# Kernel tuning notes

Hardware: AMD Instinct MI355X
Metric: run time of the kernel (lower is better)

The kernel has to match this reference:

```python
import jax, jax.numpy as jnp
import numpy as np

DIM=2048; NH=16; QK_NOPE=128; QK_ROPE=64; QK_HD=QK_NOPE+QK_ROPE; V_HD=128
Q_LORA=1536; KV_LORA=512
IDX_NH=16; IDX_HD=128; IDX_TOPK=1024
B=1; S=2048
NEG=-1e30  # finite stand-in for -inf mask

def _hadamard(n):
    H=np.array([[1.0]],dtype=np.float32)
    while H.shape[0]<n:
        H=np.block([[H,H],[H,-H]])
    return H
_H=jnp.asarray(_hadamard(IDX_HD),jnp.bfloat16)  # symmetric Sylvester Hadamard

def _rope_tables(s,d):
    inv=1.0/(10000.0**(np.arange(0,d,2)/float(d)))
    ang=np.outer(np.arange(s),inv)
    return jnp.asarray(np.cos(ang),jnp.float32),jnp.asarray(np.sin(ang),jnp.float32)

def _rope_interleaved(x,cos,sin):
    # pairs (x[2i], x[2i+1]); x: (b,s,h,d), cos/sin: (s,d//2)
    x1=x[...,0::2]; x2=x[...,1::2]
    c=cos[None,:,None,:]; s_=sin[None,:,None,:]
    return jnp.stack([x1*c-x2*s_,x1*s_+x2*c],axis=-1).reshape(x.shape)

def _rope_half(x,cos,sin):
    # non-interleaved: pairs (x[i], x[i+d/2])
    d=x.shape[-1]//2
    x1=x[...,:d]; x2=x[...,d:]
    c=cos[None,:,None,:]; s_=sin[None,:,None,:]
    return jnp.concatenate([x1*c-x2*s_,x1*s_+x2*c],axis=-1)

def _rms(x,w,eps=1e-6):
    xf=x.astype(jnp.float32)
    xf=xf*jax.lax.rsqrt(jnp.mean(xf*xf,axis=-1,keepdims=True)+eps)
    return (w*xf).astype(x.dtype)

def _ln(x,w,b,eps=1e-6):
    xf=x.astype(jnp.float32)
    mu=jnp.mean(xf,axis=-1,keepdims=True)
    var=jnp.mean((xf-mu)**2,axis=-1,keepdims=True)
    return ((xf-mu)*jax.lax.rsqrt(var+eps)*w+b).astype(x.dtype)

def _rotate(x):
    # rotate_activation: bf16 Hadamard transform, x @ H * d^-0.5 (H symmetric)
    return (x.astype(jnp.bfloat16)@_H)*(IDX_HD**-0.5)

def _forward(x,start_pos,freqs_cos,freqs_sin,mask,q_a_proj,q_a_ln_w,q_b_proj,kv_a_proj,kv_a_ln_w,kv_b_proj,o_proj,idx_wq_b,idx_wk,idx_knorm_w,idx_knorm_b,idx_weights_proj):
    b,s,_=x.shape  # start_pos==0 prefill -> cache slice == current k/kv
    sm_scale=QK_HD**-0.5
    qr=_rms(x@q_a_proj.T,q_a_ln_w)                       # (b,s,q_lora)
    q=(qr@q_b_proj.T).reshape(b,s,NH,QK_HD)
    q_nope=q[...,:QK_NOPE]
    q_pe=_rope_interleaved(q[...,QK_NOPE:],freqs_cos,freqs_sin)
    kvp=x@kv_a_proj.T
    kv=_rms(kvp[...,:KV_LORA],kv_a_ln_w)                 # latent kv cache (b,t,c)
    k_pe=_rope_interleaved(kvp[...,KV_LORA:][:,:,None,:],freqs_cos,freqs_sin)[:,:,0,:]
    # ---------- Indexer ----------
    iq=(qr@idx_wq_b.T).reshape(b,s,IDX_NH,IDX_HD)
    iq=jnp.concatenate([_rope_half(iq[...,:QK_ROPE],freqs_cos,freqs_sin),iq[...,QK_ROPE:]],axis=-1)
    ik=_ln(x@idx_wk.T,idx_knorm_w,idx_knorm_b)           # (b,s,IDX_HD)
    ik=jnp.concatenate([_rope_half(ik[:,:,None,:QK_ROPE],freqs_cos,freqs_sin)[:,:,0,:],ik[...,QK_ROPE:]],axis=-1)
    iq=_rotate(iq); ik=_rotate(ik)                       # bf16 Hadamard-rotated
    iw=(x@idx_weights_proj.T)*(IDX_NH**-0.5)             # (b,s,hI)
    wq=(iw[...,None]*iq.astype(jnp.float32)*(IDX_HD**-0.5)).astype(jnp.bfloat16)
    sc=jnp.einsum('bshd,btd->bsht',wq,ik,preferred_element_type=jnp.float32)
    index_score=jax.nn.relu(sc).sum(axis=2)+mask[None]   # bf16_index: relu, head-sum
    _,topk=jax.lax.top_k(index_score,min(IDX_TOPK,s))    # (b,s,K)
    imask=jnp.full((b,s,s),jnp.float32(NEG))
    imask=imask.at[jnp.arange(b)[:,None,None],jnp.arange(s)[None,:,None],topk].set(0.0)
    imask=imask+mask[None]
    # ---------- Latent attention (absorbed) ----------
    wkv=kv_b_proj.reshape(NH,QK_NOPE+V_HD,KV_LORA)
    q_abs=jnp.einsum('bshd,hdc->bshc',q_nope,wkv[:,:QK_NOPE])
    scores=(jnp.einsum('bshc,btc->bsht',q_abs,kv)+jnp.einsum('bshr,btr->bsht',q_pe,k_pe))*sm_scale
    scores=scores+imask[:,:,None,:]
    p=jax.nn.softmax(scores.astype(jnp.float32),axis=-1).astype(x.dtype)
    o=jnp.einsum('bsht,btc->bshc',p,kv)
    o=jnp.einsum('bshc,hdc->bshd',o,wkv[:,QK_NOPE:])
    return o.reshape(b,s,NH*V_HD)@o_proj.T

def setup_inputs():
    key=jax.random.key(0)
    ks=jax.random.split(key,10)
    def w(k,shape):
        return jax.random.normal(k,shape,jnp.float32)*(shape[-1]**-0.5)
    cos,sin=_rope_tables(S,QK_ROPE)
    causal=jnp.where(jnp.triu(jnp.ones((S,S),bool),1),jnp.float32(NEG),jnp.float32(0.0))
    return {
        'x':jax.random.normal(ks[0],(B,S,DIM),jnp.float32),
        'start_pos':0,
        'freqs_cos':cos,'freqs_sin':sin,'mask':causal,
        'q_a_proj':w(ks[1],(Q_LORA,DIM)),
        'q_a_ln_w':jnp.ones((Q_LORA,),jnp.float32),
        'q_b_proj':w(ks[2],(NH*QK_HD,Q_LORA)),
        'kv_a_proj':w(ks[3],(KV_LORA+QK_ROPE,DIM)),
        'kv_a_ln_w':jnp.ones((KV_LORA,),jnp.float32),
        'kv_b_proj':w(ks[4],(NH*(QK_NOPE+V_HD),KV_LORA)),
        'o_proj':w(ks[5],(DIM,NH*V_HD)),
        'idx_wq_b':w(ks[6],(IDX_NH*IDX_HD,Q_LORA)),
        'idx_wk':w(ks[7],(IDX_HD,DIM)),
        'idx_knorm_w':jnp.ones((IDX_HD,),jnp.float32),
        'idx_knorm_b':jnp.zeros((IDX_HD,),jnp.float32),
        'idx_weights_proj':w(ks[8],(IDX_NH,DIM)),
    }

def reference(x,start_pos,freqs_cos,freqs_sin,mask,q_a_proj,q_a_ln_w,q_b_proj,kv_a_proj,kv_a_ln_w,kv_b_proj,o_proj,idx_wq_b,idx_wk,idx_knorm_w,idx_knorm_b,idx_weights_proj):
    return _forward(x,start_pos,freqs_cos,freqs_sin,mask,q_a_proj,q_a_ln_w,q_b_proj,kv_a_proj,kv_a_ln_w,kv_b_proj,o_proj,idx_wq_b,idx_wk,idx_knorm_w,idx_knorm_b,idx_weights_proj)
```

## Files before the change

### kernel.cpp

```cpp
#include <hip/hip_runtime.h>
#include <hip/hip_bf16.h>
#include <math.h>

#define S 2048
#define NH 16
#define DIM 2048
#define QK_NOPE 128
#define QK_ROPE 64
#define QK_HD 192
#define V_HD 128
#define Q_LORA 1536
#define KV_LORA 512
#define IDX_HD 128
#define SM_SCALE 0.07216878364870323f
#define SCHUNK 512
#define PADK 40
#define XPLD 2256
#define QLD 5120
#define XPLD_PAD 2304

typedef __hip_bfloat16 bf16;
typedef unsigned short ushort_t;
typedef __attribute__((ext_vector_type(8))) short short8;
typedef __attribute__((ext_vector_type(4))) float f32x4;

__device__ __forceinline__ f32x4 mfma_bf16(short8 a, short8 b, f32x4 c) {
    return __builtin_amdgcn_mfma_f32_16x16x32_bf16(a, b, c, 0, 0, 0);
}
__device__ __forceinline__ void async16(const void* g, void* l) {
    __builtin_amdgcn_global_load_lds((const __attribute__((address_space(1))) void*)g,
                                     (__attribute__((address_space(3))) void*)l, 16, 0, 0);
}
__device__ __forceinline__ unsigned short f2bf(float f) {
    unsigned int u = __float_as_uint(f);
    return (unsigned short)((u + 0x7fff + ((u >> 16) & 1)) >> 16);
}
__device__ __forceinline__ float bf2f(unsigned short b) {
    return __uint_as_float(((unsigned int)b) << 16);
}

__global__ __launch_bounds__(256) void split_kernel(const float* __restrict__ in, ushort_t* __restrict__ hi,
                                                    ushort_t* __restrict__ lo, int n4) {
    int idx = blockIdx.x * 256 + threadIdx.x;
    if (idx >= n4) return;
    float4 v = ((const float4*)in)[idx];
    ushort4 h, l;
    h.x = f2bf(v.x); l.x = f2bf(v.x - bf2f(h.x));
    h.y = f2bf(v.y); l.y = f2bf(v.y - bf2f(h.y));
    h.z = f2bf(v.z); l.z = f2bf(v.z - bf2f(h.z));
    h.w = f2bf(v.w); l.w = f2bf(v.w - bf2f(h.w));
    ((ushort4*)hi)[idx] = h;
    ((ushort4*)lo)[idx] = l;
}

__global__ __launch_bounds__(256) void splitw2_kernel(const float* __restrict__ kv_b,
                                                      ushort_t* __restrict__ w2h, ushort_t* __restrict__ w2l) {
    int idx = blockIdx.x * 256 + threadIdx.x;
    int h = idx >> 14, rem = idx & 16383;
    int row = rem >> 7, c4 = (rem & 127) * 4;
    float4 v = *(const float4*)(kv_b + ((size_t)(h * 256 + 128 + row)) * 512 + c4);
    ushort4 hh, ll;
    hh.x = f2bf(v.x); ll.x = f2bf(v.x - bf2f(hh.x));
    hh.y = f2bf(v.y); ll.y = f2bf(v.y - bf2f(hh.y));
    hh.z = f2bf(v.z); ll.z = f2bf(v.z - bf2f(hh.z));
    hh.w = f2bf(v.w); ll.w = f2bf(v.w - bf2f(hh.w));
    *(ushort4*)(w2h + ((size_t)(h * 128 + row)) * 512 + c4) = hh;
    *(ushort4*)(w2l + ((size_t)(h * 128 + row)) * 512 + c4) = ll;
}

__global__ __launch_bounds__(256) void gemm3_lds(const ushort_t* __restrict__ Ah, const ushort_t* __restrict__ Al,
                                                 const ushort_t* __restrict__ Bh, const ushort_t* __restrict__ Bl,
                                                 float* __restrict__ C, int M, int N, int K) {
    __shared__ ushort_t sAh[128 * 32], sAl[128 * 32], sBh[128 * 32], sBl[128 * 32];
    const int tid = threadIdx.x;
    const int bm = blockIdx.y * 128, bn = blockIdx.x * 128;
    const int w = tid >> 6, lane = tid & 63;
    const int wm = (w >> 1) * 64, wn = (w & 1) * 64;
    const int fr = lane & 15, fk = (lane >> 4) * 8;
    const int srow = tid >> 2, skc = (tid & 3) * 8;
    f32x4 acc[4][4];
    for (int i = 0; i < 4; ++i)
        for (int j = 0; j < 4; ++j) acc[i][j] = f32x4{0.f, 0.f, 0.f, 0.f};
    const ushort_t* pAh0 = Ah + (size_t)(bm + srow) * K + skc;
    const ushort_t* pAh1 = Ah + (size_t)(bm + 64 + srow) * K + skc;
    const ushort_t* pAl0 = Al + (size_t)(bm + srow) * K + skc;
    const ushort_t* pAl1 = Al + (size_t)(bm + 64 + srow) * K + skc;
    const ushort_t* pBh0 = Bh + (size_t)(bn + srow) * K + skc;
    const ushort_t* pBh1 = Bh + (size_t)(bn + 64 + srow) * K + skc;
    const ushort_t* pBl0 = Bl + (size_t)(bn + srow) * K + skc;
    const ushort_t* pBl1 = Bl + (size_t)(bn + 64 + srow) * K + skc;
    ushort_t* dA0 = &sAh[srow * 32 + skc];
    ushort_t* dA1 = &sAh[(64 + srow) * 32 + skc];
    ushort_t* dAl0 = &sAl[srow * 32 + skc];
    ushort_t* dAl1 = &sAl[(64 + srow) * 32 + skc];
    ushort_t* dB0 = &sBh[srow * 32 + skc];
    ushort_t* dB1 = &sBh[(64 + srow) * 32 + skc];
    ushort_t* dBl0 = &sBl[srow * 32 + skc];
    ushort_t* dBl1 = &sBl[(64 + srow) * 32 + skc];
    for (int k0 = 0; k0 < K; k0 += 32) {
        __syncthreads();
        async16(pAh0, dA0);  async16(pAh1, dA1);
        async16(pAl0, dAl0); async16(pAl1, dAl1);
        async16(pBh0, dB0);  async16(pBh1, dB1);
        async16(pBl0, dBl0); async16(pBl1, dBl1);
        pAh0 += 32; pAh1 += 32; pAl0 += 32; pAl1 += 32;
        pBh0 += 32; pBh1 += 32; pBl0 += 32; pBl1 += 32;
        __syncthreads();
        short8 ahf[4], alf[4], bhf[4], blf[4];
        for (int i = 0; i < 4; ++i) {
            int ro = (wm + i * 16 + fr) * 32 + fk;
            ahf[i] = *(const short8*)&sAh[ro];
            alf[i] = *(const short8*)&sAl[ro];
        }
        for (int j = 0; j < 4; ++j) {
            int ro = (wn + j * 16 + fr) * 32 + fk;
            bhf[j] = *(const short8*)&sBh[ro];
            blf[j] = *(const short8*)&sBl[ro];
        }
        for (int i = 0; i < 4; ++i)
            for (int j = 0; j < 4; ++j) {
                acc[i][j] = mfma_bf16(ahf[i], bhf[j], acc[i][j]);
                acc[i][j] = mfma_bf16(ahf[i], blf[j], acc[i][j]);
                acc[i][j] = mfma_bf16(alf[i], bhf[j], acc[i][j]);
            }
    }
    const int cr = (lane >> 4) * 4, cc = lane & 15;
    for (int i = 0; i < 4; ++i)
        for (int j = 0; j < 4; ++j) {
            int row = bm + wm + i * 16 + cr;
            int col = bn + wn + j * 16 + cc;
            if (col < N)
                for (int r = 0; r < 4; ++r)
                    C[(size_t)(row + r) * N + col] = acc[i][j][r];
        }
}

__global__ __launch_bounds__(256) void rms_kernel(const float* __restrict__ in, float* __restrict__ out,
                                                  const float* __restrict__ w, int C, int ldin, int ldout) {
    const int row = blockIdx.x;
    const float* xr = in + (size_t)row * ldin;
    float* yr = out + (size_t)row * ldout;
    float ss = 0.f;
    for (int c = threadIdx.x; c < C; c += 256) { float v = xr[c]; ss += v * v; }
    for (int o = 32; o; o >>= 1) ss += __shfl_down(ss, o, 64);
    __shared__ float red[4];
    const int wave = threadIdx.x >> 6, lane = threadIdx.x & 63;
    if (lane == 0) red[wave] = ss;
    __syncthreads();
    const float tot = red[0] + red[1] + red[2] + red[3];
    const float scale = rsqrtf(tot / (float)C + 1e-6f);
    for (int c = threadIdx.x; c < C; c += 256) yr[c] = w[c] * (xr[c] * scale);
}

__global__ __launch_bounds__(256) void rms_split_kernel(const float* __restrict__ in, ushort_t* __restrict__ hi,
                                                        ushort_t* __restrict__ lo, const float* __restrict__ w,
                                                        int C, int ldin) {
    const int row = blockIdx.x;
    const float* xr = in + (size_t)row * ldin;
    float ss = 0.f;
    for (int c = threadIdx.x; c < C; c += 256) { float v = xr[c]; ss += v * v; }
    for (int o = 32; o; o >>= 1) ss += __shfl_down(ss, o, 64);
    __shared__ float red[4];
    const int wave = threadIdx.x >> 6, lane = threadIdx.x & 63;
    if (lane == 0) red[wave] = ss;
    __syncthreads();
    const float tot = red[0] + red[1] + red[2] + red[3];
    const float scale = rsqrtf(tot / (float)C + 1e-6f);
    for (int c = threadIdx.x; c < C; c += 256) {
        float v = w[c] * (xr[c] * scale);
        unsigned short h = f2bf(v);
        hi[(size_t)row * C + c] = h;
        lo[(size_t)row * C + c] = f2bf(v - bf2f(h));
    }
}

__global__ __launch_bounds__(128) void ln_kernel(float* __restrict__ x, const float* __restrict__ w,
                                                 const float* __restrict__ b, int ld) {
    const int row = blockIdx.x;
    float* xr = x + (size_t)row * ld;
    const int tid = threadIdx.x;
    float v = xr[tid];
    float sm = v;
    for (int o = 32; o; o >>= 1) sm += __shfl_down(sm, o, 64);
    __shared__ float red[2];
    if ((tid & 63) == 0) red[tid >> 6] = sm;
    __syncthreads();
    const float mu = (red[0] + red[1]) * (1.f / 128.f);
    __syncthreads();
    float d = v - mu;
    float sv = d * d;
    for (int o = 32; o; o >>= 1) sv += __shfl_down(sv, o, 64);
    if ((tid & 63) == 0) red[tid >> 6] = sv;
    __syncthreads();
    const float var = (red[0] + red[1]) * (1.f / 128.f);
    const float rs = rsqrtf(var + 1e-6f);
    xr[tid] = (v - mu) * rs * w[tid] + b[tid];
}

__global__ __launch_bounds__(256) void rope_inter_kernel(float* __restrict__ X, const float* __restrict__ ct,
                                                         const float* __restrict__ st, int H, int hs, int off,
                                                         int ld) {
    int idx = blockIdx.x * 256 + threadIdx.x;
    int k = idx & 31;
    int h = (idx >> 5) % H;
    int s = idx / (32 * H);
    if (s >= S) return;
    float c = ct[s * 32 + k], sn = st[s * 32 + k];
    float* p = X + (size_t)s * ld + h * hs + off;
    float x1 = p[2 * k], x2 = p[2 * k + 1];
    p[2 * k]     = x1 * c - x2 * sn;
    p[2 * k + 1] = x1 * sn + x2 * c;
}

__global__ __launch_bounds__(256) void rope_half_kernel(float* __restrict__ X, const float* __restrict__ ct,
                                                        const float* __restrict__ st, int H, int hs, int ld,
                                                        int soff) {
    int idx = blockIdx.x * 256 + threadIdx.x;
    int k = idx & 31;
    int h = (idx >> 5) % H;
    int s = idx / (32 * H) + soff;
    if (s >= S) return;
    float c = ct[s * 32 + k], sn = st[s * 32 + k];
    float* p = X + (size_t)s * ld + h * hs;
    float x1 = p[k], x2 = p[32 + k];
    p[k]      = x1 * c - x2 * sn;
    p[32 + k] = x1 * sn + x2 * c;
}

__global__ __launch_bounds__(128) void rotate_kernel(const float* __restrict__ in, int lds, int H,
                                                     bf16* __restrict__ out, int roff) {
    __shared__ float xs[128];
    const int r = blockIdx.x + roff, j = threadIdx.x;
    const int s = r / H, h = r - s * H;
    float v = in[(size_t)s * lds + h * 128 + j];
    xs[j] = __bfloat162float(__float2bfloat16(v));
    __syncthreads();
    float acc = 0.f;
    for (int d = 0; d < 128; ++d) {
        float xv = xs[d];
        acc += (__popc(d & j) & 1) ? -xv : xv;
    }
    float t = __bfloat162float(__float2bfloat16(acc)) * 0.08838834764831845f;
    out[(size_t)r * 128 + j] = __float2bfloat16(t);
}

__global__ __launch_bounds__(256) void wq_kernel(const float* __restrict__ iwb, bf16* __restrict__ iqr,
                                                 int ioff) {
    int idx = blockIdx.x * 256 + threadIdx.x + ioff;
    int s = idx >> 11, h = (idx >> 7) & 15;
    float a = 0.25f * iwb[(size_t)s * XPLD + h];
    float v = __bfloat162float(iqr[idx]);
    float t = (a * v) * 0.08838834764831845f;
    iqr[idx] = __float2bfloat16(t);
}

__global__ __launch_bounds__(256) void iscore_mfma(const bf16* __restrict__ wq, const bf16* __restrict__ ik,
                                                   float* __restrict__ out) {
    if (blockIdx.x > blockIdx.y + 8) return;
    __shared__ unsigned short As[128 * 32], Bs[128 * 32];
    const int bs = (blockIdx.y + 8) * 128, bt = blockIdx.x * 128;
    const int tid = threadIdx.x, w = tid >> 6, lane = tid & 63;
    const int wm = (w >> 1) * 64, wn = (w & 1) * 64;
    const int fr = lane & 15, fk = (lane >> 4) * 8;
    const int srow = lane >> 2, skc = (lane & 3) * 8;
    f32x4 sum[4][4];
    for (int i = 0; i < 4; ++i)
        for (int j = 0; j < 4; ++j) sum[i][j] = f32x4{0.f, 0.f, 0.f, 0.f};
    for (int h = 0; h < 16; ++h) {
        f32x4 acc[4][4];
        for (int i = 0; i < 4; ++i)
            for (int j = 0; j < 4; ++j) acc[i][j] = f32x4{0.f, 0.f, 0.f, 0.f};
        for (int k0 = 0; k0 < 128; k0 += 32) {
            __syncthreads();
            for (int i = 0; i < 2; ++i) {
                int seg = i * 4 + w;
                async16(wq + (size_t)(bs + seg * 16 + srow) * 2048 + h * 128 + k0 + skc, &As[seg * 512]);
                async16(ik + (size_t)(bt + seg * 16 + srow) * 128 + k0 + skc, &Bs[seg * 512]);
            }
            __syncthreads();
            short8 af[4], bff[4];
            for (int i = 0; i < 4; ++i) af[i]  = *(const short8*)&As[(wm + i * 16 + fr) * 32 + fk];
            for (int j = 0; j < 4; ++j) bff[j] = *(const short8*)&Bs[(wn + j * 16 + fr) * 32 + fk];
            for (int i = 0; i < 4; ++i)
                for (int j = 0; j < 4; ++j)
                    acc[i][j] = mfma_bf16(af[i], bff[j], acc[i][j]);
        }
        for (int i = 0; i < 4; ++i)
            for (int j = 0; j < 4; ++j)
                for (int r = 0; r < 4; ++r)
                    sum[i][j][r] += fmaxf(acc[i][j][r], 0.f);
    }
    const int cr = (lane >> 4) * 4, cc = lane & 15;
    for (int i = 0; i < 4; ++i)
        for (int j = 0; j < 4; ++j)
            for (int r = 0; r < 4; ++r)
                out[(size_t)(bs + wm + i * 16 + cr + r) * 2048 + bt + wn + j * 16 + cc] = sum[i][j][r];
}

__global__ __launch_bounds__(256) void topk_kernel(const float* __restrict__ isc, int* __restrict__ tk,
                                                   int s0) {
    __shared__ unsigned long long keys[2048];
    const int s = s0 + blockIdx.x;
    const float* row = isc + (size_t)s * 2048;
    for (int t = threadIdx.x; t < 2048; t += 256) {
        unsigned long long kk = 0ull;
        if (t <= s) {
            unsigned int vb = __float_as_uint(row[t]);
            kk = ((unsigned long long)vb << 32) | (unsigned int)(2048 - t);
        }
        keys[t] = kk;
    }
    __syncthreads();
    for (int k = 2; k <= 2048; k <<= 1) {
        for (int j = k >> 1; j > 0; j >>= 1) {
            for (int t = threadIdx.x; t < 2048; t += 256) {
                int l = t ^ j;
                if (l > t) {
                    bool up = ((t & k) == 0);
                    unsigned long long a = keys[t], b = keys[l];
                    bool sw = up ? (a < b) : (a > b);
                    if (sw) { keys[t] = b; keys[l] = a; }
                }
            }
            __syncthreads();
        }
    }
    const int cnt = min(1024, s + 1);
    for (int i = threadIdx.x; i < 1024; i += 256) {
        int t = (i < cnt) ? (2048 - (int)(keys[i] & 0xFFFFFFFFull)) : -1;
        tk[(size_t)s * 1024 + i] = t;
    }
}

__global__ __launch_bounds__(256) void w1t_kernel(const float* __restrict__ kv_b, float* __restrict__ w1t) {
    __shared__ float ts[64][65];
    const int cb = blockIdx.x * 64, db = blockIdx.y * 64, h = blockIdx.z;
    const int t = threadIdx.x;
    for (int it = 0; it < 16; ++it) {
        int idx = it * 256 + t;
        int rr = idx >> 6, cc = idx & 63;
        ts[rr][cc] = kv_b[(size_t)(h * 256 + db + rr) * 512 + cb + cc];
    }
    __syncthreads();
    for (int it = 0; it < 16; ++it) {
        int idx = it * 256 + t;
        int rr = idx >> 6, cc = idx & 63;
        w1t[(size_t)h * 65536 + (size_t)(cb + rr) * 128 + db + cc] = ts[cc][rr];
    }
}

__global__ __launch_bounds__(576) void kvsplit_kernel(const float* __restrict__ kv, const float* __restrict__ kpe,
                                                      ushort_t* __restrict__ kvh, ushort_t* __restrict__ kvl,
                                                      unsigned int* __restrict__ kvi) {
    const int t = blockIdx.x, c = threadIdx.x;
    float v = (c < 512) ? kv[(size_t)t * 512 + c] : kpe[(size_t)t * XPLD + c];
    unsigned short hi = f2bf(v);
    unsigned short lo = f2bf(v - bf2f(hi));
    kvh[(size_t)t * 576 + c] = hi;
    kvl[(size_t)t * 576 + c] = lo;
    if (c < 512) kvi[(size_t)t * 512 + c] = (unsigned int)hi | ((unsigned int)lo << 16);
}

__global__ __launch_bounds__(256) void qabs_mfma(const float* __restrict__ q, const float* __restrict__ w1t,
                                                 ushort_t* __restrict__ qah, ushort_t* __restrict__ qal) {
    __shared__ unsigned short Ah[128 * PADK], Al[128 * PADK], Bh[128 * PADK], Bl[128 * PADK];
    const int tid = threadIdx.x;
    const int bn = blockIdx.x * 128, bm = blockIdx.y * 128, h = blockIdx.z;
    const int w = tid >> 6, lane = tid & 63;
    const int wm = (w >> 1) * 64, wn = (w & 1) * 64;
    const int fr = lane & 15, fk = (lane >> 4) * 8;
    f32x4 acc[4][4];
    for (int i = 0; i < 4; ++i)
        for (int j = 0; j < 4; ++j) acc[i][j] = f32x4{0.f, 0.f, 0.f, 0.f};
    for (int k0 = 0; k0 < 128; k0 += 32) {
        __syncthreads();
        for (int it = 0; it < 4; ++it) {
            int f = it * 256 + tid;
            int row = f >> 3, kc = (f & 7) * 4;
            float4 av = *(const float4*)(q + (size_t)(bm + row) * QLD + h * QK_HD + k0 + kc);
            float4 bv = *(const float4*)(w1t + (size_t)h * 65536 + (size_t)(bn + row) * 128 + k0 + kc);
            ushort4 ahi, alo, bhi, blo;
            ahi.x = f2bf(av.x); alo.x = f2bf(av.x - bf2f(ahi.x));
            ahi.y = f2bf(av.y); alo.y = f2bf(av.y - bf2f(ahi.y));
            ahi.z = f2bf(av.z); alo.z = f2bf(av.z - bf2f(ahi.z));
            ahi.w = f2bf(av.w); alo.w = f2bf(av.w - bf2f(ahi.w));
            bhi.x = f2bf(bv.x); blo.x = f2bf(bv.x - bf2f(bhi.x));
            bhi.y = f2bf(bv.y); blo.y = f2bf(bv.y - bf2f(bhi.y));
            bhi.z = f2bf(bv.z); blo.z = f2bf(bv.z - bf2f(bhi.z));
            bhi.w = f2bf(bv.w); blo.w = f2bf(bv.w - bf2f(bhi.w));
            *(ushort4*)&Ah[row * PADK + kc] = ahi;
            *(ushort4*)&Al[row * PADK + kc] = alo;
            *(ushort4*)&Bh[row * PADK + kc] = bhi;
            *(ushort4*)&Bl[row * PADK + kc] = blo;
        }
        __syncthreads();
        short8 ahf[4], alf[4], bhf[4], blf[4];
        for (int i = 0; i < 4; ++i) {
            int ro = (wm + i * 16 + fr) * PADK + fk;
            ahf[i] = *(const short8*)&Ah[ro];
            alf[i] = *(const short8*)&Al[ro];
        }
        for (int j = 0; j < 4; ++j) {
            int ro = (wn + j * 16 + fr) * PADK + fk;
            bhf[j] = *(const short8*)&Bh[ro];
            blf[j] = *(const short8*)&Bl[ro];
        }
        for (int i = 0; i < 4; ++i)
            for (int j = 0; j < 4; ++j) {
                acc[i][j] = mfma_bf16(ahf[i], bhf[j], acc[i][j]);
                acc[i][j] = mfma_bf16(ahf[i], blf[j], acc[i][j]);
                acc[i][j] = mfma_bf16(alf[i], bhf[j], acc[i][j]);
            }
    }
    const int cr = (lane >> 4) * 4, cc = lane & 15;
    for (int i = 0; i < 4; ++i)
        for (int j = 0; j < 4; ++j)
            for (int r = 0; r < 4; ++r) {
                int srow = bm + wm + i * 16 + cr + r;
                int col = bn + wn + j * 16 + cc;
                float f = acc[i][j][r] * SM_SCALE;
                size_t addr = ((size_t)srow * 16 + h) * 576 + col;
                unsigned short hi = f2bf(f);
                qah[addr] = hi;
                qal[addr] = f2bf(f - bf2f(hi));
            }
}

__global__ __launch_bounds__(256) void qpe_split(const float* __restrict__ q, ushort_t* __restrict__ qah,
                                                 ushort_t* __restrict__ qal) {
    int idx = blockIdx.x * 256 + threadIdx.x;
    int r = idx & 63, h = (idx >> 6) & 15, s = idx >> 10;
    float f = q[(size_t)s * QLD + h * QK_HD + 128 + r] * SM_SCALE;
    size_t addr = ((size_t)s * 16 + h) * 576 + 512 + r;
    unsigned short hi = f2bf(f);
    qah[addr] = hi;
    qal[addr] = f2bf(f - bf2f(hi));
}

__global__ __launch_bounds__(512) void attn_score_mfma(const ushort_t* __restrict__ qah,
                                                       const ushort_t* __restrict__ qal,
                                                       const ushort_t* __restrict__ kvh,
                                                       const ushort_t* __restrict__ kvl,
                                                       const int* __restrict__ tk,
                                                       float* __restrict__ scb, int s0, int dense) {
    const int sl = blockIdx.x, s = s0 + sl, pass = blockIdx.y;
    const int tid = threadIdx.x, w = tid >> 6, lane = tid & 63;
    const int cnt = min(1024, s + 1);
    if (pass * 256 >= cnt) {
        for (int i = tid; i < 4096; i += 512) {
            int head = i >> 8, key = i & 255;
            scb[((size_t)sl * 16 + head) * 1024 + pass * 256 + key] = -1e30f;
        }
        return;
    }
    __shared__ int tks[256];
    __shared__ __align__(16) ushort_t kh[2][8192], kl[2][8192];
    if (tid < 256) {
        if (dense) {
            tks[tid] = pass * 256 + tid;
        } else {
            int t = tk[(size_t)s * 1024 + pass * 256 + tid];
            tks[tid] = t < 0 ? 0 : t;
        }
    }
    __syncthreads();
    const int fr = lane & 15, g = lane >> 4;
    const size_t abase = ((size_t)s * 16 + fr) * 576 + g * 8;
    const int R0 = tid >> 2;
    const int sw = (tid & 3) ^ ((R0 >> 1) & 3);
    const size_t t0 = (size_t)tks[R0], t1 = (size_t)tks[R0 + 128];
    const ushort_t* gh0 = kvh + t0 * 576 + sw * 8;
    const ushort_t* gh1 = kvh + t1 * 576 + sw * 8;
    const ushort_t* gl0 = kvl + t0 * 576 + sw * 8;
    const ushort_t* gl1 = kvl + t1 * 576 + sw * 8;
    const int ro_a = (w * 32 + fr) * 32 + ((g ^ ((fr >> 1) & 3)) << 3);
    async16(gh0, &kh[0][w * 512]);
    async16(gh1, &kh[0][4096 + w * 512]);
    async16(gl0, &kl[0][w * 512]);
    async16(gl1, &kl[0][4096 + w * 512]);
    short8 qh = *(const short8*)(qah + abase);
    short8 ql = *(const short8*)(qal + abase);
    f32x4 acc0 = {0.f, 0.f, 0.f, 0.f}, acc1 = {0.f, 0.f, 0.f, 0.f};
    int cur = 0;
    __syncthreads();
    for (int ch = 0; ch < 18; ++ch) {
        if (ch < 17) {
            int off = (ch + 1) * 32;
            async16(gh0 + off, &kh[cur ^ 1][w * 512]);
            async16(gh1 + off, &kh[cur ^ 1][4096 + w * 512]);
            async16(gl0 + off, &kl[cur ^ 1][w * 512]);
            async16(gl1 + off, &kl[cur ^ 1][4096 + w * 512]);
        }
        short8 qhc = qh, qlc = ql;
        if (ch < 17) {
            qh = *(const short8*)(qah + abase + (ch + 1) * 32);
            ql = *(const short8*)(qal + abase + (ch + 1) * 32);
        }
        short8 bh0 = *(const short8*)&kh[cur][ro_a];
        short8 bl0 = *(const short8*)&kl[cur][ro_a];
        short8 bh1 = *(const short8*)&kh[cur][ro_a + 512];
        short8 bl1 = *(const short8*)&kl[cur][ro_a + 512];
        acc0 = mfma_bf16(qhc, bh0, acc0);
        acc0 = mfma_bf16(qhc, bl0, acc0);
        acc0 = mfma_bf16(qlc, bh0, acc0);
        acc1 = mfma_bf16(qhc, bh1, acc1);
        acc1 = mfma_bf16(qhc, bl1, acc1);
        acc1 = mfma_bf16(qlc, bh1, acc1);
        __syncthreads();
        cur ^= 1;
    }
    const int cr = (lane >> 4) * 4, cc = lane & 15;
    for (int r = 0; r < 4; ++r) {
        int head = cr + r;
        int key0 = pass * 256 + w * 32 + cc;
        int key1 = key0 + 16;
        scb[((size_t)sl * 16 + head) * 1024 + key0] = (key0 < cnt) ? acc0[r] : -1e30f;
        scb[((size_t)sl * 16 + head) * 1024 + key1] = (key1 < cnt) ? acc1[r] : -1e30f;
    }
}

__global__ __launch_bounds__(256) void softmax_pb(const float* __restrict__ scb,
                                                  ushort_t* __restrict__ pbh, ushort_t* __restrict__ pbl) {
    const size_t row = blockIdx.x;
    const float* src = scb + row * 1024;
    const int tid = threadIdx.x, wave = tid >> 6, lane = tid & 63;
    __shared__ float red[4];
    float v[4];
    float m = -INFINITY;
    for (int i = 0; i < 4; ++i) { v[i] = src[tid + 256 * i]; m = fmaxf(m, v[i]); }
    for (int o = 32; o; o >>= 1) m = fmaxf(m, __shfl_down(m, o, 64));
    if (lane == 0) red[wave] = m;
    __syncthreads();
    m = fmaxf(fmaxf(red[0], red[1]), fmaxf(red[2], red[3]));
    __syncthreads();
    float e[4], l = 0.f;
    for (int i = 0; i < 4; ++i) { e[i] = __expf(v[i] - m); l += e[i]; }
    for (int o = 32; o; o >>= 1) l += __shfl_down(l, o, 64);
    if (lane == 0) red[wave] = l;
    __syncthreads();
    const float il = 1.f / (red[0] + red[1] + red[2] + red[3]);
    for (int i = 0; i < 4; ++i) {
        float p = e[i] * il;
        unsigned short hi = f2bf(p);
        pbh[row * 1024 + tid + 256 * i] = hi;
        pbl[row * 1024 + tid + 256 * i] = f2bf(p - bf2f(hi));
    }
}

#define PV_GATHER(KC)                                                                    \
    g0 = *(const uint4*)(kvi + (size_t)tks[(KC) * 32 + r0     ] * 512 + gp4);            \
    g1 = *(const uint4*)(kvi + (size_t)tks[(KC) * 32 + r0 + 4 ] * 512 + gp4);            \
    g2 = *(const uint4*)(kvi + (size_t)tks[(KC) * 32 + r0 + 8 ] * 512 + gp4);            \
    g3 = *(const uint4*)(kvi + (size_t)tks[(KC) * 32 + r0 + 12] * 512 + gp4);            \
    g4 = *(const uint4*)(kvi + (size_t)tks[(KC) * 32 + r0 + 16] * 512 + gp4);            \
    g5 = *(const uint4*)(kvi + (size_t)tks[(KC) * 32 + r0 + 20] * 512 + gp4);            \
    g6 = *(const uint4*)(kvi + (size_t)tks[(KC) * 32 + r0 + 24] * 512 + gp4);            \
    g7 = *(const uint4*)(kvi + (size_t)tks[(KC) * 32 + r0 + 28] * 512 + gp4);
#define PV_STORE()                                                                       \
    *(uint4*)&vt[(r0     ) * 512 + ((gp ^ 0) << 2)] = g0;                                \
    *(uint4*)&vt[(r0 + 4 ) * 512 + ((gp ^ 0) << 2)] = g1;                                \
    *(uint4*)&vt[(r0 + 8 ) * 512 + ((gp ^ 2) << 2)] = g2;                                \
    *(uint4*)&vt[(r0 + 12) * 512 + ((gp ^ 2) << 2)] = g3;                                \
    *(uint4*)&vt[(r0 + 16) * 512 + ((gp ^ 4) << 2)] = g4;                                \
    *(uint4*)&vt[(r0 + 20) * 512 + ((gp ^ 4) << 2)] = g5;                                \
    *(uint4*)&vt[(r0 + 24) * 512 + ((gp ^ 6) << 2)] = g6;                                \
    *(uint4*)&vt[(r0 + 28) * 512 + ((gp ^ 6) << 2)] = g7;
__global__ __launch_bounds__(512) void attn_pv_mfma(const ushort_t* __restrict__ pbh,
                                                    const ushort_t* __restrict__ pbl,
                                                    const unsigned int* __restrict__ kvi,
                                                    const int* __restrict__ tk,
                                                    ushort_t* __restrict__ o1h, ushort_t* __restrict__ o1l,
                                                    int s0, int dense) {
    const int sl = blockIdx.x, s = s0 + sl;
    const int tid = threadIdx.x, w = tid >> 6, lane = tid & 63;
    __shared__ int tks[1024];
    __shared__ unsigned int vt[32 * 512];
    for (int j = tid; j < 1024; j += 512) {
        if (dense) {
            tks[j] = j;
        } else {
            int t = tk[(size_t)s * 1024 + j];
            tks[j] = t < 0 ? 0 : t;
        }
    }
    const int fr = lane & 15, g = lane >> 4, fko = g * 8;
    const int r0 = tid >> 7;
    const int gp = tid & 127;
    const int gp4 = gp * 4;
    f32x4 acc[4];
    for (int i = 0; i < 4; ++i) acc[i] = f32x4{0.f, 0.f, 0.f, 0.f};
    const size_t pbase = ((size_t)sl * 16 + fr) * 1024 + fko;
    uint4 g0, g1, g2, g3, g4, g5, g6, g7;
    __syncthreads();
    PV_GATHER(0)
    PV_STORE()
    __syncthreads();
    for (int kc = 0; kc < 32; ++kc) {
        if (kc < 31) {
            PV_GATHER(kc + 1)
        }
        short8 ph = *(const short8*)(pbh + pbase + kc * 32);
        short8 pl = *(const short8*)(pbl + pbase + kc * 32);
        #pragma unroll
        for (int sub = 0; sub < 4; ++sub) {
            const int cb = (w * 64 + sub * 16 + fr) ^ (g << 3);
            short8 bh, bl;
            #pragma unroll
            for (int jj = 0; jj < 8; ++jj) {
                const unsigned int v = vt[(fko + jj) * 512 + cb];
                bh[jj] = (short)(v & 0xffffu);
                bl[jj] = (short)(v >> 16);
            }
            acc[sub] = mfma_bf16(ph, bh, acc[sub]);
            acc[sub] = mfma_bf16(pl, bh, acc[sub]);
            acc[sub] = mfma_bf16(ph, bl, acc[sub]);
        }
        __syncthreads();
        if (kc < 31) {
            PV_STORE()
            __syncthreads();
        }
    }
    const int cr = (lane >> 4) * 4, cc = lane & 15;
    for (int sub = 0; sub < 4; ++sub)
        for (int r = 0; r < 4; ++r) {
            int head = cr + r, c = w * 64 + sub * 16 + cc;
            float f = acc[sub][r];
            unsigned short hv = f2bf(f);
            size_t addr = ((size_t)sl * 16 + head) * 512 + c;
            o1h[addr] = hv;
            o1l[addr] = f2bf(f - bf2f(hv));
        }
}

__global__ __launch_bounds__(256) void outproj_mfma(const ushort_t* __restrict__ o1h,
                                                    const ushort_t* __restrict__ o1l,
                                                    const ushort_t* __restrict__ w2h,
                                                    const ushort_t* __restrict__ w2l,
                                                    ushort_t* __restrict__ o2h, ushort_t* __restrict__ o2l,
                                                    int s0) {
    __shared__ ushort_t sAh[128 * 32], sAl[128 * 32], sBh[128 * 32], sBl[128 * 32];
    const int tid = threadIdx.x;
    const int bm = blockIdx.x * 128, h = blockIdx.y;
    const int w = tid >> 6, lane = tid & 63;
    const int wm = (w >> 1) * 64, wn = (w & 1) * 64;
    const int fr = lane & 15, fk = (lane >> 4) * 8;
    const int srow = tid >> 2, skc = (tid & 3) * 8;
    f32x4 acc[4][4];
    for (int i = 0; i < 4; ++i)
        for (int j = 0; j < 4; ++j) acc[i][j] = f32x4{0.f, 0.f, 0.f, 0.f};
    const ushort_t* pAh0 = o1h + ((size_t)(bm + srow) * 16 + h) * 512 + skc;
    const ushort_t* pAh1 = o1h + ((size_t)(bm + 64 + srow) * 16 + h) * 512 + skc;
    const ushort_t* pAl0 = o1l + ((size_t)(bm + srow) * 16 + h) * 512 + skc;
    const ushort_t* pAl1 = o1l + ((size_t)(bm + 64 + srow) * 16 + h) * 512 + skc;
    const ushort_t* pBh0 = w2h + ((size_t)(h * 128 + srow)) * 512 + skc;
    const ushort_t* pBh1 = w2h + ((size_t)(h * 128 + 64 + srow)) * 512 + skc;
    const ushort_t* pBl0 = w2l + ((size_t)(h * 128 + srow)) * 512 + skc;
    const ushort_t* pBl1 = w2l + ((size_t)(h * 128 + 64 + srow)) * 512 + skc;
    ushort_t* dA0 = &sAh[srow * 32 + skc];
    ushort_t* dA1 = &sAh[(64 + srow) * 32 + skc];
    ushort_t* dAl0 = &sAl[srow * 32 + skc];
    ushort_t* dAl1 = &sAl[(64 + srow) * 32 + skc];
    ushort_t* dB0 = &sBh[srow * 32 + skc];
    ushort_t* dB1 = &sBh[(64 + srow) * 32 + skc];
    ushort_t* dBl0 = &sBl[srow * 32 + skc];
    ushort_t* dBl1 = &sBl[(64 + srow) * 32 + skc];
    for (int k0 = 0; k0 < 512; k0 += 32) {
        __syncthreads();
        async16(pAh0, dA0);  async16(pAh1, dA1);
        async16(pAl0, dAl0); async16(pAl1, dAl1);
        async16(pBh0, dB0);  async16(pBh1, dB1);
        async16(pBl0, dBl0); async16(pBl1, dBl1);
        pAh0 += 32; pAh1 += 32; pAl0 += 32; pAl1 += 32;
        pBh0 += 32; pBh1 += 32; pBl0 += 32; pBl1 += 32;
        __syncthreads();
        short8 ahf[4], alf[4], bhf[4], blf[4];
        for (int i = 0; i < 4; ++i) {
            int ro = (wm + i * 16 + fr) * 32 + fk;
            ahf[i] = *(const short8*)&sAh[ro];
            alf[i] = *(const short8*)&sAl[ro];
        }
        for (int j = 0; j < 4; ++j) {
            int ro = (wn + j * 16 + fr) * 32 + fk;
            bhf[j] = *(const short8*)&sBh[ro];
            blf[j] = *(const short8*)&sBl[ro];
        }
        for (int i = 0; i < 4; ++i)
            for (int j = 0; j < 4; ++j) {
                acc[i][j] = mfma_bf16(ahf[i], bhf[j], acc[i][j]);
                acc[i][j] = mfma_bf16(ahf[i], blf[j], acc[i][j]);
                acc[i][j] = mfma_bf16(alf[i], bhf[j], acc[i][j]);
            }
    }
    const int cr = (lane >> 4) * 4, cc = lane & 15;
    for (int i = 0; i < 4; ++i)
        for (int j = 0; j < 4; ++j)
            for (int r = 0; r < 4; ++r) {
                int srow2 = s0 + bm + wm + i * 16 + cr + r;
                int col = wn + j * 16 + cc;
                size_t addr = (size_t)srow2 * 2048 + h * 128 + col;
                float f = acc[i][j][r];
                unsigned short hv = f2bf(f);
                o2h[addr] = hv;
                o2l[addr] = f2bf(f - bf2f(hv));
            }
}

extern "C" void kernel_launch(void* const* d_in, const int* in_sizes, int n_in,
                              void* d_out, int out_size, void* d_ws, size_t ws_size,
                              hipStream_t stream) {
    const float* x         = (const float*)d_in[0];
    const float* fcos      = (const float*)d_in[2];
    const float* fsin      = (const float*)d_in[3];
    const float* q_a_proj  = (const float*)d_in[5];
    const float* q_a_ln_w  = (const float*)d_in[6];
    const float* q_b_proj  = (const float*)d_in[7];
    const float* kv_a_proj = (const float*)d_in[8];
    const float* kv_a_ln_w = (const float*)d_in[9];
    const float* kv_b      = (const float*)d_in[10];
    const float* o_proj    = (const float*)d_in[11];
    const float* idx_wq_b  = (const float*)d_in[12];
    const float* idx_wk    = (const float*)d_in[13];
    const float* iknw      = (const float*)d_in[14];
    const float* iknb      = (const float*)d_in[15];
    const float* idx_wp    = (const float*)d_in[16];
    float* out = (float*)d_out;

    char* ws = (char*)d_ws;
    size_t off = 0;
    auto alloc = [&](size_t bytes) {
        char* p = ws + off;
        off += (bytes + 255) & ~(size_t)255;
        return p;
    };
    float* xp  = (float*)alloc((size_t)S * XPLD * 4);
    ushort_t* qrh = (ushort_t*)alloc((size_t)S * Q_LORA * 2);
    ushort_t* qrl = (ushort_t*)alloc((size_t)S * Q_LORA * 2);
    float* qib = (float*)alloc((size_t)S * QLD * 4);
    char* RAt  = alloc(31457280);
    float* isc = (float*)RAt;
    bf16* iqr  = (bf16*)(RAt + 16777216);
    bf16* ikr  = (bf16*)(RAt + 16777216 + 8388608);
    ushort_t* xh = (ushort_t*)RAt;
    ushort_t* xl = xh + (size_t)S * DIM;
    ushort_t* wq2h = (ushort_t*)RAt;
    ushort_t* wq2l = wq2h + (size_t)5120 * Q_LORA;
    float* w1t = (float*)RAt;
    ushort_t* wpackh = (ushort_t*)qib;
    ushort_t* wpackl = wpackh + (size_t)XPLD_PAD * DIM;
    char* kvtail = RAt + (size_t)22 * 1024 * 1024;
    unsigned int* kvi = (unsigned int*)kvtail;
    ushort_t* w2h = (ushort_t*)(kvtail + (size_t)4 * 1024 * 1024);
    ushort_t* w2l = w2h + (size_t)16 * 128 * 512;
    const size_t CHUNK_BYTES = (size_t)SCHUNK * 16 * 1024 * 4 + (size_t)SCHUNK * 16 * 1024 * 2 * 2
                             + (size_t)SCHUNK * 16 * 512 * 4;
    if (off < CHUNK_BYTES) off = (CHUNK_BYTES + 255) & ~(size_t)255;
    int* tk        = (int*)alloc((size_t)S * 1024 * 4);
    float* kv      = (float*)alloc((size_t)S * KV_LORA * 4);
    ushort_t* o2h  = (ushort_t*)alloc((size_t)S * 2048 * 2);
    ushort_t* o2l  = (ushort_t*)alloc((size_t)S * 2048 * 2);
    ushort_t* qah  = (ushort_t*)alloc((size_t)S * 16 * 576 * 2);
    ushort_t* qal  = (ushort_t*)alloc((size_t)S * 16 * 576 * 2);
    ushort_t* kvh  = (ushort_t*)alloc((size_t)S * 576 * 2);
    ushort_t* kvl  = (ushort_t*)alloc((size_t)S * 576 * 2);
    float* scb    = (float*)ws;
    ushort_t* pbh = (ushort_t*)(ws + (size_t)SCHUNK * 16 * 1024 * 4);
    ushort_t* pbl = pbh + (size_t)SCHUNK * 16 * 1024;
    ushort_t* o1h = (ushort_t*)(ws + (size_t)SCHUNK * 16 * 1024 * 8);
    ushort_t* o1l = o1h + (size_t)SCHUNK * 16 * 512;
    ushort_t* oph = (ushort_t*)ws;
    ushort_t* opl = oph + (size_t)DIM * 2048;

    split_kernel<<<S * DIM / 1024, 256, 0, stream>>>(x, xh, xl, S * DIM / 4);
    split_kernel<<<Q_LORA * DIM / 1024, 256, 0, stream>>>(q_a_proj, wpackh, wpackl, Q_LORA * DIM / 4);
    split_kernel<<<576 * DIM / 1024, 256, 0, stream>>>(kv_a_proj, wpackh + (size_t)1536 * DIM,
                                                       wpackl + (size_t)1536 * DIM, 576 * DIM / 4);
    split_kernel<<<128 * DIM / 1024, 256, 0, stream>>>(idx_wk, wpackh + (size_t)2112 * DIM,
                                                       wpackl + (size_t)2112 * DIM, 128 * DIM / 4);
    split_kernel<<<16 * DIM / 1024, 256, 0, stream>>>(idx_wp, wpackh + (size_t)2240 * DIM,
                                                      wpackl + (size_t)2240 * DIM, 16 * DIM / 4);
    hipMemsetAsync(wpackh + (size_t)XPLD * DIM, 0, (size_t)(XPLD_PAD - XPLD) * DIM * 2, stream);
    hipMemsetAsync(wpackl + (size_t)XPLD * DIM, 0, (size_t)(XPLD_PAD - XPLD) * DIM * 2, stream);
    gemm3_lds<<<dim3((XPLD + 127) / 128, S / 128), 256, 0, stream>>>(xh, xl, wpackh, wpackl, xp, S, XPLD, DIM);
    rms_split_kernel<<<S, 256, 0, stream>>>(xp, qrh, qrl, q_a_ln_w, Q_LORA, XPLD);
    rms_kernel<<<S, 256, 0, stream>>>(xp + 1536, kv, kv_a_ln_w, KV_LORA, XPLD, KV_LORA);
    split_kernel<<<3072 * Q_LORA / 1024, 256, 0, stream>>>(q_b_proj, wq2h, wq2l, 3072 * Q_LORA / 4);
    split_kernel<<<2048 * Q_LORA / 1024, 256, 0, stream>>>(idx_wq_b, wq2h + (size_t)3072 * Q_LORA,
                                                           wq2l + (size_t)3072 * Q_LORA, 2048 * Q_LORA / 4);
    gemm3_lds<<<dim3(QLD / 128, S / 128), 256, 0, stream>>>(qrh, qrl, wq2h, wq2l, qib, S, QLD, Q_LORA);
    rope_inter_kernel<<<S * NH * 32 / 256, 256, 0, stream>>>(qib, fcos, fsin, NH, QK_HD, QK_NOPE, QLD);
    rope_inter_kernel<<<S * 32 / 256, 256, 0, stream>>>(xp + 1536, fcos, fsin, 1, 0, KV_LORA, XPLD);
    rope_half_kernel<<<S * NH * 32 / 512, 256, 0, stream>>>(qib + 3072, fcos, fsin, NH, 128, QLD, 1024);
    ln_kernel<<<S, 128, 0, stream>>>(xp + 2112, iknw, iknb, XPLD);
    rope_half_kernel<<<S * 32 / 256, 256, 0, stream>>>(xp + 2112, fcos, fsin, 1, 0, XPLD, 0);
    rotate_kernel<<<S * NH / 2, 128, 0, stream>>>(qib + 3072, QLD, NH, iqr, 1024 * NH);
    rotate_kernel<<<S, 128, 0, stream>>>(xp + 2112, XPLD, 1, ikr, 0);
    wq_kernel<<<S * NH * 128 / 512, 256, 0, stream>>>(xp + 2240, iqr, 1024 * NH * 128);
    iscore_mfma<<<dim3(16, 8), 256, 0, stream>>>(iqr, ikr, isc);
    topk_kernel<<<1024, 256, 0, stream>>>(isc, tk, 1024);
    w1t_kernel<<<dim3(8, 2, 16), 256, 0, stream>>>(kv_b, w1t);
    qabs_mfma<<<dim3(4, S / 128, 16), 256, 0, stream>>>(qib, w1t, qah, qal);
    qpe_split<<<S * NH * 64 / 256, 256, 0, stream>>>(qib, qah, qal);
    kvsplit_kernel<<<S, 576, 0, stream>>>(kv, xp + 1536, kvh, kvl, kvi);
    splitw2_kernel<<<1024, 256, 0, stream>>>(kv_b, w2h, w2l);
    for (int c = 0; c < 4; ++c) {
        int s0 = c * SCHUNK;
        int dense = (c < 2) ? 1 : 0;
        attn_score_mfma<<<dim3(SCHUNK, 4), 512, 0, stream>>>(qah, qal, kvh, kvl, tk, scb, s0, dense);
        softmax_pb<<<SCHUNK * 16, 256, 0, stream>>>(scb, pbh, pbl);
        attn_pv_mfma<<<SCHUNK, 512, 0, stream>>>(pbh, pbl, kvi, tk, o1h, o1l, s0, dense);
        outproj_mfma<<<dim3(4, 16), 256, 0, stream>>>(o1h, o1l, w2h, w2l, o2h, o2l, s0);
    }
    split_kernel<<<DIM * 2048 / 1024, 256, 0, stream>>>(o_proj, oph, opl, DIM * 2048 / 4);
    gemm3_lds<<<dim3(DIM / 128, S / 128), 256, 0, stream>>>(o2h, o2l, oph, opl, out, S, DIM, NH * V_HD);
}
```

Before: 1.515 ms.

## Make attention score tile loads wave-private and drop block barriers

Each wave now loads only the 32 keys it consumes into its own slice of shared memory, with the key indices read straight from global instead of staged through a shared index table. Because no data crosses waves, the per-chunk __syncthreads is replaced by explicit s_waitcnt vmcnt counters and scheduling barriers. This removes 18 block-wide barriers per block and lets waves progress independently. The cost is correctness risk: it depends on exact vmcnt accounting (the 6 outstanding loads include the two q loads) and on there being no WAR hazard on the double buffer without a barrier.

```diff
diff --git a/kernel.cpp b/kernel.cpp
--- a/kernel.cpp
+++ b/kernel.cpp
@@ -437,6 +437,11 @@
     qal[addr] = f2bf(f - bf2f(hi));
 }
 
+#define SC_STAGE(BUF, O)                                    \
+    async16(gha + (O), &kh[BUF][w * 1024]);                 \
+    async16(ghb + (O), &kh[BUF][w * 1024 + 512]);           \
+    async16(gla + (O), &kl[BUF][w * 1024]);                 \
+    async16(glb + (O), &kl[BUF][w * 1024 + 512]);
 __global__ __launch_bounds__(512) void attn_score_mfma(const ushort_t* __restrict__ qah,
                                                        const ushort_t* __restrict__ qal,
                                                        const ushort_t* __restrict__ kvh,
@@ -453,61 +458,63 @@
         }
         return;
     }
-    __shared__ int tks[256];
     __shared__ __align__(16) ushort_t kh[2][8192], kl[2][8192];
-    if (tid < 256) {
-        if (dense) {
-            tks[tid] = pass * 256 + tid;
-        } else {
-            int t = tk[(size_t)s * 1024 + pass * 256 + tid];
-            tks[tid] = t < 0 ? 0 : t;
-        }
-    }
-    __syncthreads();
+    const int rloc = lane >> 2;
+    int t_a, t_b;
+    if (dense) {
+        t_a = pass * 256 + w * 32 + rloc;
+        t_b = t_a + 16;
+    } else {
+        int ta = tk[(size_t)s * 1024 + pass * 256 + w * 32 + rloc];
+        int tb = tk[(size_t)s * 1024 + pass * 256 + w * 32 + 16 + rloc];
+        t_a = ta < 0 ? 0 : ta;
+        t_b = tb < 0 ? 0 : tb;
+    }
+    const int swg = (lane & 3) ^ ((lane >> 3) & 3);
+    const ushort_t* gha = kvh + (size_t)t_a * 576 + swg * 8;
+    const ushort_t* ghb = kvh + (size_t)t_b * 576 + swg * 8;
+    const ushort_t* gla = kvl + (size_t)t_a * 576 + swg * 8;
+    const ushort_t* glb = kvl + (size_t)t_b * 576 + swg * 8;
     const int fr = lane & 15, g = lane >> 4;
     const size_t abase = ((size_t)s * 16 + fr) * 576 + g * 8;
-    const int R0 = tid >> 2;
-    const int sw = (tid & 3) ^ ((R0 >> 1) & 3);
-    const size_t t0 = (size_t)tks[R0], t1 = (size_t)tks[R0 + 128];
-    const ushort_t* gh0 = kvh + t0 * 576 + sw * 8;
-    const ushort_t* gh1 = kvh + t1 * 576 + sw * 8;
-    const ushort_t* gl0 = kvl + t0 * 576 + sw * 8;
-    const ushort_t* gl1 = kvl + t1 * 576 + sw * 8;
-    const int ro_a = (w * 32 + fr) * 32 + ((g ^ ((fr >> 1) & 3)) << 3);
-    async16(gh0, &kh[0][w * 512]);
-    async16(gh1, &kh[0][4096 + w * 512]);
-    async16(gl0, &kl[0][w * 512]);
-    async16(gl1, &kl[0][4096 + w * 512]);
+    const int ro0 = w * 1024 + fr * 32 + ((g ^ ((fr >> 1) & 3)) << 3);
+    const int ro1 = ro0 + 512;
+    f32x4 acc0 = {0.f, 0.f, 0.f, 0.f}, acc1 = {0.f, 0.f, 0.f, 0.f};
+    SC_STAGE(0, 0)
     short8 qh = *(const short8*)(qah + abase);
     short8 ql = *(const short8*)(qal + abase);
-    f32x4 acc0 = {0.f, 0.f, 0.f, 0.f}, acc1 = {0.f, 0.f, 0.f, 0.f};
-    int cur = 0;
-    __syncthreads();
-    for (int ch = 0; ch < 18; ++ch) {
-        if (ch < 17) {
-            int off = (ch + 1) * 32;
-            async16(gh0 + off, &kh[cur ^ 1][w * 512]);
-            async16(gh1 + off, &kh[cur ^ 1][4096 + w * 512]);
-            async16(gl0 + off, &kl[cur ^ 1][w * 512]);
-            async16(gl1 + off, &kl[cur ^ 1][4096 + w * 512]);
-        }
-        short8 qhc = qh, qlc = ql;
-        if (ch < 17) {
-            qh = *(const short8*)(qah + abase + (ch + 1) * 32);
-            ql = *(const short8*)(qal + abase + (ch + 1) * 32);
-        }
-        short8 bh0 = *(const short8*)&kh[cur][ro_a];
-        short8 bl0 = *(const short8*)&kl[cur][ro_a];
-        short8 bh1 = *(const short8*)&kh[cur][ro_a + 512];
-        short8 bl1 = *(const short8*)&kl[cur][ro_a + 512];
-        acc0 = mfma_bf16(qhc, bh0, acc0);
-        acc0 = mfma_bf16(qhc, bl0, acc0);
-        acc0 = mfma_bf16(qlc, bh0, acc0);
-        acc1 = mfma_bf16(qhc, bh1, acc1);
-        acc1 = mfma_bf16(qhc, bl1, acc1);
-        acc1 = mfma_bf16(qlc, bh1, acc1);
-        __syncthreads();
-        cur ^= 1;
+    for (int ch = 0; ch < 17; ++ch) {
+        const int cur = ch & 1;
+        SC_STAGE(cur ^ 1, (ch + 1) * 32)
+        short8 qhn = *(const short8*)(qah + abase + (ch + 1) * 32);
+        short8 qln = *(const short8*)(qal + abase + (ch + 1) * 32);
+        asm volatile("s_waitcnt vmcnt(6)" ::: "memory");
+        __builtin_amdgcn_sched_barrier(0);
+        short8 bh0 = *(const short8*)&kh[cur][ro0];
+        short8 bl0 = *(const short8*)&kl[cur][ro0];
+        short8 bh1 = *(const short8*)&kh[cur][ro1];
+        short8 bl1 = *(const short8*)&kl[cur][ro1];
+        acc0 = mfma_bf16(qh, bh0, acc0);
+        acc0 = mfma_bf16(qh, bl0, acc0);
+        acc0 = mfma_bf16(ql, bh0, acc0);
+        acc1 = mfma_bf16(qh, bh1, acc1);
+        acc1 = mfma_bf16(qh, bl1, acc1);
+        acc1 = mfma_bf16(ql, bh1, acc1);
+        qh = qhn; ql = qln;
+    }
+    {
+        asm volatile("s_waitcnt vmcnt(0)" ::: "memory");
+        __builtin_amdgcn_sched_barrier(0);
+        short8 bh0 = *(const short8*)&kh[1][ro0];
+        short8 bl0 = *(const short8*)&kl[1][ro0];
+        short8 bh1 = *(const short8*)&kh[1][ro1];
+        short8 bl1 = *(const short8*)&kl[1][ro1];
+        acc0 = mfma_bf16(qh, bh0, acc0);
+        acc0 = mfma_bf16(qh, bl0, acc0);
+        acc0 = mfma_bf16(ql, bh0, acc0);
+        acc1 = mfma_bf16(qh, bh1, acc1);
+        acc1 = mfma_bf16(qh, bl1, acc1);
+        acc1 = mfma_bf16(ql, bh1, acc1);
     }
     const int cr = (lane >> 4) * 4, cc = lane & 15;
     for (int r = 0; r < 4; ++r) {
```

Result: no change. 1.512 ms (-0.2%).
